# Kernel tuning notes

Hardware: AMD Instinct MI355X
Metric: run time of the kernel (lower is better)

The kernel has to match this reference:

```python
import jax, jax.numpy as jnp
import numpy as np

NUM_HEADS = 1
LN_EPS = 1e-5


def setup_inputs() -> dict:
    key = jax.random.key(0)
    ks = jax.random.split(key, 4)
    B, N, C = 16, 128 * 128 + 1, 64
    x = jax.random.normal(ks[0], (B, N, C), dtype=jnp.float32)
    Wq = jax.random.normal(ks[1], (C, C), dtype=jnp.float32) * 0.02
    Wkv = jax.random.normal(ks[2], (C, 2 * C), dtype=jnp.float32) * 0.02
    ln_g = jnp.ones((C,), dtype=jnp.float32)
    ln_b = jnp.zeros((C,), dtype=jnp.float32)
    Wp = jax.random.normal(ks[3], (C, C), dtype=jnp.float32) * 0.02
    bp = jnp.zeros((C,), dtype=jnp.float32)
    return {"x": x, "Wq": Wq, "Wkv": Wkv, "ln_g": ln_g, "ln_b": ln_b,
            "Wp": Wp, "bp": bp, "H": 128, "W": 128}


def _layernorm(x, g, b):
    mu = x.mean(-1, keepdims=True)
    var = ((x - mu) ** 2).mean(-1, keepdims=True)
    return (x - mu) * jax.lax.rsqrt(var + LN_EPS) * g + b


def reference(x, Wq, Wkv, ln_g, ln_b, Wp, bp, H, W):
    B, N, C = x.shape
    h = NUM_HEADS
    d = C // h
    scale = d ** (-0.5)

    # remove weight token
    tokens = x[:, 1:, :]          # [B, N-1, C]
    wt = x[:, :1, :]              # [B, 1, C]

    # mask-gated selection: feat @ wt_token^T -> sigmoid -> binary mask
    mask_weight = jnp.einsum('bnc,bmc->bnm', tokens, wt)   # [B, N-1, 1]
    mask_prob = jax.nn.sigmoid(mask_weight)
    mask = (mask_prob > 0.5).astype(x.dtype)
    mask_count = mask.sum(axis=(1, 2))                      # [B]
    # if a batch element has an all-zero mask, set it to all-ones
    mask = jnp.where((mask_count == 0)[:, None, None], jnp.ones_like(mask), mask)

    # queries over the full sequence (with wt token)
    q = (x @ Wq).reshape(B, N, h, d).transpose(0, 2, 1, 3)  # [B, h, N, d]

    # simFeats_fusion: masked weighted-sum pooling into 2 tokens
    x_po_f = (tokens * mask * (mask_weight * mask)).sum(axis=1, keepdims=True)        # [B,1,C]
    x_ne_f = (tokens * (1 - mask) * (mask_weight * (1 - mask))).sum(axis=1, keepdims=True)
    x_ = jnp.concatenate([wt, x_po_f, x_ne_f], axis=1)      # [B, 3, C]
    x_ = _layernorm(x_, ln_g, ln_b)

    kv = (x_ @ Wkv).reshape(B, 3, 2, h, d).transpose(2, 0, 3, 1, 4)  # [2, B, h, 3, d]
    k, v = kv[0], kv[1]

    attn = jnp.einsum('bhnd,bhmd->bhnm', q, k) * scale       # [B, h, N, 3]
    attn = jax.nn.softmax(attn, axis=-1)
    out = jnp.einsum('bhnm,bhmd->bhnd', attn, v)             # [B, h, N, d]
    out = out.transpose(0, 2, 1, 3).reshape(B, N, C)
    out = out @ Wp + bp
    return (out, mask, mask_prob)
```

## Files before the change

kernel.cpp:

```cpp
#include <hip/hip_runtime.h>
#include <cstddef>

#define BB 16
#define NN 16385
#define NT 16384
#define CC 64
#define P1B 64
#define P3B 64

typedef __attribute__((ext_vector_type(4))) float f4;

__global__ __launch_bounds__(256) void k_p1(
    const float* __restrict__ x, const float* __restrict__ Wq,
    const float* __restrict__ Wkv, const float* __restrict__ Wp,
    float* __restrict__ mask_out, float* __restrict__ prob_out,
    float* __restrict__ po_part, float* __restrict__ ne_part,
    float* __restrict__ cnt_part,
    float* __restrict__ M2t, float* __restrict__ M3)
{
  const int b = blockIdx.y, bx = blockIdx.x;
  const int tid = threadIdx.x, lane = tid & 63, wave = tid >> 6;

  if (b == BB) {
    const int c = bx, j = lane, q = wave;
    float s2 = 0.f, s3 = 0.f;
    #pragma unroll
    for (int dd = 0; dd < 16; ++dd) {
      const int d = q * 16 + dd;
      s2 += Wq[j * 64 + d] * Wkv[c * 128 + d];
      s3 += Wkv[c * 128 + 64 + d] * Wp[d * 64 + j];
    }
    __shared__ float t2[4][64], t3[4][64];
    t2[q][j] = s2; t3[q][j] = s3;
    __syncthreads();
    if (q == 0) {
      M2t[c * 64 + j] = t2[0][j] + t2[1][j] + t2[2][j] + t2[3][j];
      M3 [c * 64 + j] = t3[0][j] + t3[1][j] + t3[2][j] + t3[3][j];
    }
    return;
  }

  const int g = lane & 15, t = lane >> 4, c0 = g * 4;
  const float* xb = x + (size_t)b * NN * CC;
  const f4 wt4 = *reinterpret_cast<const f4*>(xb + c0);

  float apo[4] = {0.f, 0.f, 0.f, 0.f};
  float ane4[4] = {0.f, 0.f, 0.f, 0.f};
  float cntl = 0.f;

  for (int grp = bx * 4 + wave; grp < NT / 4; grp += P1B * 4) {
    const int n0 = grp * 4;
    const f4 xv = *reinterpret_cast<const f4*>(xb + (size_t)(1 + n0 + t) * CC + c0);
    float p = xv.x * wt4.x + xv.y * wt4.y + xv.z * wt4.z + xv.w * wt4.w;
    p += __shfl_xor(p, 1);
    p += __shfl_xor(p, 2);
    p += __shfl_xor(p, 4);
    p += __shfl_xor(p, 8);
    const bool m = p > 0.f;
    const float po = m ? p : 0.f;
    const float ne = m ? 0.f : p;
    apo[0] += po * xv.x; apo[1] += po * xv.y; apo[2] += po * xv.z; apo[3] += po * xv.w;
    ane4[0] += ne * xv.x; ane4[1] += ne * xv.y; ane4[2] += ne * xv.z; ane4[3] += ne * xv.w;
    if (g == 0) {
      const int nt = n0 + t;
      mask_out[(size_t)b * NT + nt] = m ? 1.f : 0.f;
      prob_out[(size_t)b * NT + nt] = 1.f / (1.f + __expf(-p));
      if (m) cntl += 1.f;
    }
  }

  #pragma unroll
  for (int i = 0; i < 4; ++i) {
    apo[i] += __shfl_xor(apo[i], 16); apo[i] += __shfl_xor(apo[i], 32);
    ane4[i] += __shfl_xor(ane4[i], 16); ane4[i] += __shfl_xor(ane4[i], 32);
  }
  cntl += __shfl_xor(cntl, 16);
  cntl += __shfl_xor(cntl, 32);

  __shared__ float s_po[4][64], s_ne[4][64], s_cnt[4];
  if (t == 0) {
    #pragma unroll
    for (int i = 0; i < 4; ++i) { s_po[wave][c0 + i] = apo[i]; s_ne[wave][c0 + i] = ane4[i]; }
  }
  if (lane == 0) s_cnt[wave] = cntl;
  __syncthreads();
  if (wave == 0) {
    const float sp = s_po[0][lane] + s_po[1][lane] + s_po[2][lane] + s_po[3][lane];
    const float sn = s_ne[0][lane] + s_ne[1][lane] + s_ne[2][lane] + s_ne[3][lane];
    const size_t base = ((size_t)b * P1B + bx) * 64 + lane;
    po_part[base] = sp;
    ne_part[base] = sn;
    if (lane == 0) cnt_part[b * P1B + bx] = s_cnt[0] + s_cnt[1] + s_cnt[2] + s_cnt[3];
  }
}

__global__ __launch_bounds__(256) void k_p23(
    const float* __restrict__ x, const float* __restrict__ ln_g,
    const float* __restrict__ ln_b, const float* __restrict__ bp,
    const float* __restrict__ po_part, const float* __restrict__ ne_part,
    const float* __restrict__ cnt_part,
    const float* __restrict__ M2t, const float* __restrict__ M3,
    float* __restrict__ out, float* __restrict__ mask_out)
{
  const int b = blockIdx.y;
  const int tid = threadIdx.x, lane = tid & 63, wave = tid >> 6;
  const int j = lane, q = wave;
  const int kq = tid >> 4, jg = tid & 15;
  const float* xb = x + (size_t)b * NN * CC;

  __shared__ float s_flag;
  __shared__ f4 sm_po[16][16], sm_ne[16][16];
  __shared__ float po_s[64], ne_s[64];
  __shared__ float y[3][64];
  __shared__ float A_l[3][64], V_l[3][64];

  f4 sp4 = {0.f, 0.f, 0.f, 0.f}, sn4 = {0.f, 0.f, 0.f, 0.f};
  #pragma unroll
  for (int i = 0; i < 4; ++i) {
    const size_t base = ((size_t)b * P1B + kq + 16 * i) * 64 + jg * 4;
    const f4 a = *reinterpret_cast<const f4*>(po_part + base);
    const f4 c = *reinterpret_cast<const f4*>(ne_part + base);
    sp4 += a; sn4 += c;
  }
  sm_po[kq][jg] = sp4;
  sm_ne[kq][jg] = sn4;

  if (q == 3) {
    float cs = cnt_part[b * P1B + j];
    for (int o = 1; o < 64; o <<= 1) cs += __shfl_xor(cs, o);
    if (j == 0) s_flag = (cs == 0.f) ? 1.f : 0.f;
  }
  __syncthreads();

  if (q == 0) {
    float s1 = 0.f, s2v = 0.f;
    #pragma unroll
    for (int k = 0; k < 16; ++k) {
      s1  += sm_po[k][j >> 2][j & 3];
      s2v += sm_ne[k][j >> 2][j & 3];
    }
    po_s[j] = s1; ne_s[j] = s2v;
  }
  __syncthreads();

  const bool flag = (s_flag != 0.f);
  if (q < 3) {
    float v;
    if (q == 0)      v = xb[j];
    else if (q == 1) v = flag ? ne_s[j] : po_s[j];
    else             v = flag ? 0.f : ne_s[j];
    float s = v;
    for (int o = 1; o < 64; o <<= 1) s += __shfl_xor(s, o);
    const float mu = s * (1.f / 64.f);
    const float d = v - mu;
    float s2 = d * d;
    for (int o = 1; o < 64; o <<= 1) s2 += __shfl_xor(s2, o);
    y[q][j] = d * rsqrtf(s2 * (1.f / 64.f) + 1e-5f) * ln_g[j] + ln_b[j];
  }
  __syncthreads();

  if (q < 3) {
    float sa = 0.f, sv = 0.f;
    #pragma unroll 8
    for (int c = 0; c < 64; ++c) {
      const float yc = y[q][c];
      sa += yc * M2t[c * 64 + j];
      sv += yc * M3 [c * 64 + j];
    }
    A_l[q][j] = 0.125f * sa;
    V_l[q][j] = sv;
  }
  __syncthreads();

  const int r = lane >> 3, c0 = (lane & 7) * 8;
  const f4 A0a = *reinterpret_cast<const f4*>(&A_l[0][c0]);
  const f4 A0b = *reinterpret_cast<const f4*>(&A_l[0][c0 + 4]);
  const f4 A1a = *reinterpret_cast<const f4*>(&A_l[1][c0]);
  const f4 A1b = *reinterpret_cast<const f4*>(&A_l[1][c0 + 4]);
  const f4 A2a = *reinterpret_cast<const f4*>(&A_l[2][c0]);
  const f4 A2b = *reinterpret_cast<const f4*>(&A_l[2][c0 + 4]);
  const f4 V0a = *reinterpret_cast<const f4*>(&V_l[0][c0]);
  const f4 V0b = *reinterpret_cast<const f4*>(&V_l[0][c0 + 4]);
  const f4 V1a = *reinterpret_cast<const f4*>(&V_l[1][c0]);
  const f4 V1b = *reinterpret_cast<const f4*>(&V_l[1][c0 + 4]);
  const f4 V2a = *reinterpret_cast<const f4*>(&V_l[2][c0]);
  const f4 V2b = *reinterpret_cast<const f4*>(&V_l[2][c0 + 4]);
  const f4 BPa = *reinterpret_cast<const f4*>(bp + c0);
  const f4 BPb = *reinterpret_cast<const f4*>(bp + c0 + 4);

  if (flag) {
    for (int i = blockIdx.x * 256 + tid; i < NT; i += P3B * 256)
      mask_out[(size_t)b * NT + i] = 1.f;
  }

  float* ob = out + (size_t)b * NN * CC;

  const int ngroups = (NN + 7) / 8;
  for (int grp = blockIdx.x * 4 + wave; grp < ngroups; grp += P3B * 4) {
    const int n = grp * 8 + r;
    const bool valid = n < NN;
    f4 x0 = {0.f, 0.f, 0.f, 0.f}, x1 = {0.f, 0.f, 0.f, 0.f};
    if (valid) {
      x0 = *reinterpret_cast<const f4*>(xb + (size_t)n * CC + c0);
      x1 = *reinterpret_cast<const f4*>(xb + (size_t)n * CC + c0 + 4);
    }

    float p0 = x0.x * A0a.x + x0.y * A0a.y + x0.z * A0a.z + x0.w * A0a.w
             + x1.x * A0b.x + x1.y * A0b.y + x1.z * A0b.z + x1.w * A0b.w;
    float p1 = x0.x * A1a.x + x0.y * A1a.y + x0.z * A1a.z + x0.w * A1a.w
             + x1.x * A1b.x + x1.y * A1b.y + x1.z * A1b.z + x1.w * A1b.w;
    float p2 = x0.x * A2a.x + x0.y * A2a.y + x0.z * A2a.z + x0.w * A2a.w
             + x1.x * A2b.x + x1.y * A2b.y + x1.z * A2b.z + x1.w * A2b.w;
    #pragma unroll
    for (int o = 1; o < 8; o <<= 1) {
      p0 += __shfl_xor(p0, o);
      p1 += __shfl_xor(p1, o);
      p2 += __shfl_xor(p2, o);
    }
    const float mx = fmaxf(p0, fmaxf(p1, p2));
    float e0 = __expf(p0 - mx), e1 = __expf(p1 - mx), e2 = __expf(p2 - mx);
    const float inv = 1.f / (e0 + e1 + e2);
    e0 *= inv; e1 *= inv; e2 *= inv;

    f4 o0, o1;
    o0.x = BPa.x + e0 * V0a.x + e1 * V1a.x + e2 * V2a.x;
    o0.y = BPa.y + e0 * V0a.y + e1 * V1a.y + e2 * V2a.y;
    o0.z = BPa.z + e0 * V0a.z + e1 * V1a.z + e2 * V2a.z;
    o0.w = BPa.w + e0 * V0a.w + e1 * V1a.w + e2 * V2a.w;
    o1.x = BPb.x + e0 * V0b.x + e1 * V1b.x + e2 * V2b.x;
    o1.y = BPb.y + e0 * V0b.y + e1 * V1b.y + e2 * V2b.y;
    o1.z = BPb.z + e0 * V0b.z + e1 * V1b.z + e2 * V2b.z;
    o1.w = BPb.w + e0 * V0b.w + e1 * V1b.w + e2 * V2b.w;
    if (valid) {
      *reinterpret_cast<f4*>(ob + (size_t)n * CC + c0) = o0;
      *reinterpret_cast<f4*>(ob + (size_t)n * CC + c0 + 4) = o1;
    }
  }
}

extern "C" void kernel_launch(void* const* d_in, const int* in_sizes, int n_in,
                              void* d_out, int out_size, void* d_ws, size_t ws_size,
                              hipStream_t stream) {
  (void)in_sizes; (void)n_in; (void)out_size; (void)ws_size;
  const float* x    = (const float*)d_in[0];
  const float* Wq   = (const float*)d_in[1];
  const float* Wkv  = (const float*)d_in[2];
  const float* ln_g = (const float*)d_in[3];
  const float* ln_b = (const float*)d_in[4];
  const float* Wp   = (const float*)d_in[5];
  const float* bp   = (const float*)d_in[6];

  float* out      = (float*)d_out;
  float* mask_out = out + (size_t)BB * NN * CC;
  float* prob_out = mask_out + (size_t)BB * NT;

  float* ws        = (float*)d_ws;
  float* po_part   = ws;
  float* ne_part   = po_part + (size_t)BB * P1B * 64;
  float* cnt_part  = ne_part + (size_t)BB * P1B * 64;
  float* M2t       = cnt_part + BB * P1B;
  float* M3        = M2t + 64 * 64;

  k_p1<<<dim3(P1B, BB + 1), 256, 0, stream>>>(x, Wq, Wkv, Wp, mask_out, prob_out,
                                              po_part, ne_part, cnt_part, M2t, M3);
  k_p23<<<dim3(P3B, BB), 256, 0, stream>>>(x, ln_g, ln_b, bp,
                                           po_part, ne_part, cnt_part,
                                           M2t, M3, out, mask_out);
}
```

Measured before the change: 44.83 us.

## Fuse two phases into one cooperative kernel with a grid-wide sync

Merges the masked-pooling phase and the attention/projection phase into a single cooperative kernel that separates them with a grid barrier. The weight-product matrices are computed by designated blocks instead of an extra block row. This removes the second kernel launch and the gap between launches, and may let x stay warmer in cache for the second pass. The cost is the grid sync and a hard limit on grid size from co-residency, with a fallback to the two-kernel path if the cooperative launch fails.

```diff
diff --git a/kernel.cpp b/kernel.cpp
--- a/kernel.cpp
+++ b/kernel.cpp
@@ -1,5 +1,8 @@
 #include <hip/hip_runtime.h>
+#include <hip/hip_cooperative_groups.h>
 #include <cstddef>
+
+namespace cg = cooperative_groups;
 
 #define BB 16
 #define NN 16385
@@ -7,8 +10,227 @@
 #define CC 64
 #define P1B 64
 #define P3B 64
+#define PSTRIDE 64
 
 typedef __attribute__((ext_vector_type(4))) float f4;
+
+template <int PB>
+__global__ __launch_bounds__(256, 4) void k_fused(
+    const float* __restrict__ x, const float* __restrict__ Wq,
+    const float* __restrict__ Wkv, const float* __restrict__ ln_g,
+    const float* __restrict__ ln_b, const float* __restrict__ Wp,
+    const float* __restrict__ bp,
+    float* __restrict__ out, float* __restrict__ mask_out,
+    float* __restrict__ prob_out,
+    float* __restrict__ po_part, float* __restrict__ ne_part,
+    float* __restrict__ cnt_part,
+    float* __restrict__ M2t, float* __restrict__ M3)
+{
+  const int bid = blockIdx.x;
+  const int b = bid / PB, bx = bid % PB;
+  const int tid = threadIdx.x, lane = tid & 63, wave = tid >> 6;
+  const float* xb = x + (size_t)b * NN * CC;
+
+  __shared__ float s_po[4][64], s_ne[4][64], s_cnt[4];
+  __shared__ float s_flag;
+  __shared__ f4 sm_po[16][16], sm_ne[16][16];
+  __shared__ float po_s[64], ne_s[64];
+  __shared__ float y[3][64];
+  __shared__ float A_l[3][64], V_l[3][64];
+
+  {
+    const int g = lane & 15, t = lane >> 4, c0 = g * 4;
+    const f4 wt4 = *reinterpret_cast<const f4*>(xb + c0);
+
+    float apo[4] = {0.f, 0.f, 0.f, 0.f};
+    float ane4[4] = {0.f, 0.f, 0.f, 0.f};
+    float cntl = 0.f;
+
+    for (int grp = bx * 4 + wave; grp < NT / 4; grp += PB * 4) {
+      const int n0 = grp * 4;
+      const f4 xv = *reinterpret_cast<const f4*>(xb + (size_t)(1 + n0 + t) * CC + c0);
+      float p = xv.x * wt4.x + xv.y * wt4.y + xv.z * wt4.z + xv.w * wt4.w;
+      p += __shfl_xor(p, 1);
+      p += __shfl_xor(p, 2);
+      p += __shfl_xor(p, 4);
+      p += __shfl_xor(p, 8);
+      const bool m = p > 0.f;
+      const float po = m ? p : 0.f;
+      const float ne = m ? 0.f : p;
+      apo[0] += po * xv.x; apo[1] += po * xv.y; apo[2] += po * xv.z; apo[3] += po * xv.w;
+      ane4[0] += ne * xv.x; ane4[1] += ne * xv.y; ane4[2] += ne * xv.z; ane4[3] += ne * xv.w;
+      if (g == 0) {
+        const int nt = n0 + t;
+        mask_out[(size_t)b * NT + nt] = m ? 1.f : 0.f;
+        prob_out[(size_t)b * NT + nt] = 1.f / (1.f + __expf(-p));
+        if (m) cntl += 1.f;
+      }
+    }
+
+    #pragma unroll
+    for (int i = 0; i < 4; ++i) {
+      apo[i] += __shfl_xor(apo[i], 16); apo[i] += __shfl_xor(apo[i], 32);
+      ane4[i] += __shfl_xor(ane4[i], 16); ane4[i] += __shfl_xor(ane4[i], 32);
+    }
+    cntl += __shfl_xor(cntl, 16);
+    cntl += __shfl_xor(cntl, 32);
+
+    if (t == 0) {
+      #pragma unroll
+      for (int i = 0; i < 4; ++i) { s_po[wave][c0 + i] = apo[i]; s_ne[wave][c0 + i] = ane4[i]; }
+    }
+    if (lane == 0) s_cnt[wave] = cntl;
+    __syncthreads();
+    if (wave == 0) {
+      const float sp = s_po[0][lane] + s_po[1][lane] + s_po[2][lane] + s_po[3][lane];
+      const float sn = s_ne[0][lane] + s_ne[1][lane] + s_ne[2][lane] + s_ne[3][lane];
+      const size_t base = ((size_t)b * PSTRIDE + bx) * 64 + lane;
+      po_part[base] = sp;
+      ne_part[base] = sn;
+      if (lane == 0) cnt_part[b * PSTRIDE + bx] = s_cnt[0] + s_cnt[1] + s_cnt[2] + s_cnt[3];
+    }
+
+    if (bx == 1) {
+      const int j = tid & 63, cc = tid >> 6;
+      const int c = 4 * b + cc;
+      float s2 = 0.f, s3 = 0.f;
+      #pragma unroll 8
+      for (int d = 0; d < 64; ++d) {
+        s2 += Wq[j * 64 + d] * Wkv[c * 128 + d];
+        s3 += Wkv[c * 128 + 64 + d] * Wp[d * 64 + j];
+      }
+      M2t[c * 64 + j] = s2;
+      M3 [c * 64 + j] = s3;
+    }
+  }
+
+  cg::this_grid().sync();
+
+  const int j = lane, q = wave;
+  const int kq = tid >> 4, jg = tid & 15;
+
+  f4 sp4 = {0.f, 0.f, 0.f, 0.f}, sn4 = {0.f, 0.f, 0.f, 0.f};
+  #pragma unroll
+  for (int k = kq; k < PB; k += 16) {
+    const size_t base = ((size_t)b * PSTRIDE + k) * 64 + jg * 4;
+    sp4 += *reinterpret_cast<const f4*>(po_part + base);
+    sn4 += *reinterpret_cast<const f4*>(ne_part + base);
+  }
+  sm_po[kq][jg] = sp4;
+  sm_ne[kq][jg] = sn4;
+
+  if (q == 3) {
+    float cs = (j < PB) ? cnt_part[b * PSTRIDE + j] : 0.f;
+    for (int o = 1; o < 64; o <<= 1) cs += __shfl_xor(cs, o);
+    if (j == 0) s_flag = (cs == 0.f) ? 1.f : 0.f;
+  }
+  __syncthreads();
+
+  if (q == 0) {
+    float s1 = 0.f, s2v = 0.f;
+    #pragma unroll
+    for (int k = 0; k < 16; ++k) {
+      s1  += sm_po[k][j >> 2][j & 3];
+      s2v += sm_ne[k][j >> 2][j & 3];
+    }
+    po_s[j] = s1; ne_s[j] = s2v;
+  }
+  __syncthreads();
+
+  const bool flag = (s_flag != 0.f);
+  if (q < 3) {
+    float v;
+    if (q == 0)      v = xb[j];
+    else if (q == 1) v = flag ? ne_s[j] : po_s[j];
+    else             v = flag ? 0.f : ne_s[j];
+    float s = v;
+    for (int o = 1; o < 64; o <<= 1) s += __shfl_xor(s, o);
+    const float mu = s * (1.f / 64.f);
+    const float d = v - mu;
+    float s2 = d * d;
+    for (int o = 1; o < 64; o <<= 1) s2 += __shfl_xor(s2, o);
+    y[q][j] = d * rsqrtf(s2 * (1.f / 64.f) + 1e-5f) * ln_g[j] + ln_b[j];
+  }
+  __syncthreads();
+
+  if (q < 3) {
+    float sa = 0.f, sv = 0.f;
+    #pragma unroll 8
+    for (int c = 0; c < 64; ++c) {
+      const float yc = y[q][c];
+      sa += yc * M2t[c * 64 + j];
+      sv += yc * M3 [c * 64 + j];
+    }
+    A_l[q][j] = 0.125f * sa;
+    V_l[q][j] = sv;
+  }
+  __syncthreads();
+
+  const int r = lane >> 3, c0 = (lane & 7) * 8;
+  const f4 A0a = *reinterpret_cast<const f4*>(&A_l[0][c0]);
+  const f4 A0b = *reinterpret_cast<const f4*>(&A_l[0][c0 + 4]);
+  const f4 A1a = *reinterpret_cast<const f4*>(&A_l[1][c0]);
+  const f4 A1b = *reinterpret_cast<const f4*>(&A_l[1][c0 + 4]);
+  const f4 A2a = *reinterpret_cast<const f4*>(&A_l[2][c0]);
+  const f4 A2b = *reinterpret_cast<const f4*>(&A_l[2][c0 + 4]);
+  const f4 V0a = *reinterpret_cast<const f4*>(&V_l[0][c0]);
+  const f4 V0b = *reinterpret_cast<const f4*>(&V_l[0][c0 + 4]);
+  const f4 V1a = *reinterpret_cast<const f4*>(&V_l[1][c0]);
+  const f4 V1b = *reinterpret_cast<const f4*>(&V_l[1][c0 + 4]);
+  const f4 V2a = *reinterpret_cast<const f4*>(&V_l[2][c0]);
+  const f4 V2b = *reinterpret_cast<const f4*>(&V_l[2][c0 + 4]);
+  const f4 BPa = *reinterpret_cast<const f4*>(bp + c0);
+  const f4 BPb = *reinterpret_cast<const f4*>(bp + c0 + 4);
+
+  if (flag) {
+    for (int i = bx * 256 + tid; i < NT; i += PB * 256)
+      mask_out[(size_t)b * NT + i] = 1.f;
+  }
+
+  float* ob = out + (size_t)b * NN * CC;
+
+  const int ngroups = (NN + 7) / 8;
+  for (int grp = bx * 4 + wave; grp < ngroups; grp += PB * 4) {
+    const int n = grp * 8 + r;
+    const bool valid = n < NN;
+    f4 x0 = {0.f, 0.f, 0.f, 0.f}, x1 = {0.f, 0.f, 0.f, 0.f};
+    if (valid) {
+      const f4* p = reinterpret_cast<const f4*>(xb + (size_t)n * CC + c0);
+      x0 = p[0]; x1 = p[1];
+    }
+
+    float p0 = x0.x * A0a.x + x0.y * A0a.y + x0.z * A0a.z + x0.w * A0a.w
+             + x1.x * A0b.x + x1.y * A0b.y + x1.z * A0b.z + x1.w * A0b.w;
+    float p1 = x0.x * A1a.x + x0.y * A1a.y + x0.z * A1a.z + x0.w * A1a.w
+             + x1.x * A1b.x + x1.y * A1b.y + x1.z * A1b.z + x1.w * A1b.w;
+    float p2 = x0.x * A2a.x + x0.y * A2a.y + x0.z * A2a.z + x0.w * A2a.w
+             + x1.x * A2b.x + x1.y * A2b.y + x1.z * A2b.z + x1.w * A2b.w;
+    #pragma unroll
+    for (int o = 1; o < 8; o <<= 1) {
+      p0 += __shfl_xor(p0, o);
+      p1 += __shfl_xor(p1, o);
+      p2 += __shfl_xor(p2, o);
+    }
+    const float mx = fmaxf(p0, fmaxf(p1, p2));
+    float e0 = __expf(p0 - mx), e1 = __expf(p1 - mx), e2 = __expf(p2 - mx);
+    const float inv = 1.f / (e0 + e1 + e2);
+    e0 *= inv; e1 *= inv; e2 *= inv;
+
+    f4 o0, o1;
+    o0.x = BPa.x + e0 * V0a.x + e1 * V1a.x + e2 * V2a.x;
+    o0.y = BPa.y + e0 * V0a.y + e1 * V1a.y + e2 * V2a.y;
+    o0.z = BPa.z + e0 * V0a.z + e1 * V1a.z + e2 * V2a.z;
+    o0.w = BPa.w + e0 * V0a.w + e1 * V1a.w + e2 * V2a.w;
+    o1.x = BPb.x + e0 * V0b.x + e1 * V1b.x + e2 * V2b.x;
+    o1.y = BPb.y + e0 * V0b.y + e1 * V1b.y + e2 * V2b.y;
+    o1.z = BPb.z + e0 * V0b.z + e1 * V1b.z + e2 * V2b.z;
+    o1.w = BPb.w + e0 * V0b.w + e1 * V1b.w + e2 * V2b.w;
+    if (valid) {
+      f4* p = reinterpret_cast<f4*>(ob + (size_t)n * CC + c0);
+      p[0] = o0; p[1] = o1;
+    }
+  }
+}
 
 __global__ __launch_bounds__(256) void k_p1(
     const float* __restrict__ x, const float* __restrict__ Wq,
@@ -87,14 +309,14 @@
   if (wave == 0) {
     const float sp = s_po[0][lane] + s_po[1][lane] + s_po[2][lane] + s_po[3][lane];
     const float sn = s_ne[0][lane] + s_ne[1][lane] + s_ne[2][lane] + s_ne[3][lane];
-    const size_t base = ((size_t)b * P1B + bx) * 64 + lane;
+    const size_t base = ((size_t)b * PSTRIDE + bx) * 64 + lane;
     po_part[base] = sp;
     ne_part[base] = sn;
-    if (lane == 0) cnt_part[b * P1B + bx] = s_cnt[0] + s_cnt[1] + s_cnt[2] + s_cnt[3];
+    if (lane == 0) cnt_part[b * PSTRIDE + bx] = s_cnt[0] + s_cnt[1] + s_cnt[2] + s_cnt[3];
   }
 }
 
-__global__ __launch_bounds__(256) void k_p23(
+__global__ __launch_bounds__(256, 4) void k_p23(
     const float* __restrict__ x, const float* __restrict__ ln_g,
     const float* __restrict__ ln_b, const float* __restrict__ bp,
     const float* __restrict__ po_part, const float* __restrict__ ne_part,
@@ -117,16 +339,15 @@
   f4 sp4 = {0.f, 0.f, 0.f, 0.f}, sn4 = {0.f, 0.f, 0.f, 0.f};
   #pragma unroll
   for (int i = 0; i < 4; ++i) {
-    const size_t base = ((size_t)b * P1B + kq + 16 * i) * 64 + jg * 4;
-    const f4 a = *reinterpret_cast<const f4*>(po_part + base);
-    const f4 c = *reinterpret_cast<const f4*>(ne_part + base);
-    sp4 += a; sn4 += c;
+    const size_t base = ((size_t)b * PSTRIDE + kq + 16 * i) * 64 + jg * 4;
+    sp4 += *reinterpret_cast<const f4*>(po_part + base);
+    sn4 += *reinterpret_cast<const f4*>(ne_part + base);
   }
   sm_po[kq][jg] = sp4;
   sm_ne[kq][jg] = sn4;
 
   if (q == 3) {
-    float cs = cnt_part[b * P1B + j];
+    float cs = cnt_part[b * PSTRIDE + j];
     for (int o = 1; o < 64; o <<= 1) cs += __shfl_xor(cs, o);
     if (j == 0) s_flag = (cs == 0.f) ? 1.f : 0.f;
   }
@@ -201,8 +422,8 @@
     const bool valid = n < NN;
     f4 x0 = {0.f, 0.f, 0.f, 0.f}, x1 = {0.f, 0.f, 0.f, 0.f};
     if (valid) {
-      x0 = *reinterpret_cast<const f4*>(xb + (size_t)n * CC + c0);
-      x1 = *reinterpret_cast<const f4*>(xb + (size_t)n * CC + c0 + 4);
+      const f4* p = reinterpret_cast<const f4*>(xb + (size_t)n * CC + c0);
+      x0 = p[0]; x1 = p[1];
     }
 
     float p0 = x0.x * A0a.x + x0.y * A0a.y + x0.z * A0a.z + x0.w * A0a.w
@@ -232,8 +453,8 @@
     o1.z = BPb.z + e0 * V0b.z + e1 * V1b.z + e2 * V2b.z;
     o1.w = BPb.w + e0 * V0b.w + e1 * V1b.w + e2 * V2b.w;
     if (valid) {
-      *reinterpret_cast<f4*>(ob + (size_t)n * CC + c0) = o0;
-      *reinterpret_cast<f4*>(ob + (size_t)n * CC + c0 + 4) = o1;
+      f4* p = reinterpret_cast<f4*>(ob + (size_t)n * CC + c0);
+      p[0] = o0; p[1] = o1;
     }
   }
 }
@@ -256,14 +477,42 @@
 
   float* ws        = (float*)d_ws;
   float* po_part   = ws;
-  float* ne_part   = po_part + (size_t)BB * P1B * 64;
-  float* cnt_part  = ne_part + (size_t)BB * P1B * 64;
-  float* M2t       = cnt_part + BB * P1B;
+  float* ne_part   = po_part + (size_t)BB * PSTRIDE * 64;
+  float* cnt_part  = ne_part + (size_t)BB * PSTRIDE * 64;
+  float* M2t       = cnt_part + BB * PSTRIDE;
   float* M3        = M2t + 64 * 64;
 
-  k_p1<<<dim3(P1B, BB + 1), 256, 0, stream>>>(x, Wq, Wkv, Wp, mask_out, prob_out,
-                                              po_part, ne_part, cnt_part, M2t, M3);
-  k_p23<<<dim3(P3B, BB), 256, 0, stream>>>(x, ln_g, ln_b, bp,
-                                           po_part, ne_part, cnt_part,
-                                           M2t, M3, out, mask_out);
+  int maxBlk = 0;
+  hipError_t qerr = hipOccupancyMaxActiveBlocksPerMultiprocessor(
+      &maxBlk, (const void*)k_fused<64>, 256, 0);
+
+  bool launched = false;
+  if (qerr == hipSuccess && maxBlk >= 2) {
+    void* args[] = {
+      (void*)&x, (void*)&Wq, (void*)&Wkv, (void*)&ln_g, (void*)&ln_b,
+      (void*)&Wp, (void*)&bp, (void*)&out, (void*)&mask_out, (void*)&prob_out,
+      (void*)&po_part, (void*)&ne_part, (void*)&cnt_part, (void*)&M2t, (void*)&M3
+    };
+    hipError_t lerr;
+    if (maxBlk >= 4) {
+      lerr = hipLaunchCooperativeKernel((const void*)k_fused<64>, dim3(BB * 64),
+                                        dim3(256), args, 0, stream);
+    } else if (maxBlk == 3) {
+      lerr = hipLaunchCooperativeKernel((const void*)k_fused<48>, dim3(BB * 48),
+                                        dim3(256), args, 0, stream);
+    } else {
+      lerr = hipLaunchCooperativeKernel((const void*)k_fused<32>, dim3(BB * 32),
+                                        dim3(256), args, 0, stream);
+    }
+    launched = (lerr == hipSuccess);
+    if (!launched) (void)hipGetLastError();
+  }
+
+  if (!launched) {
+    k_p1<<<dim3(P1B, BB + 1), 256, 0, stream>>>(x, Wq, Wkv, Wp, mask_out, prob_out,
+                                                po_part, ne_part, cnt_part, M2t, M3);
+    k_p23<<<dim3(P3B, BB), 256, 0, stream>>>(x, ln_g, ln_b, bp,
+                                             po_part, ne_part, cnt_part,
+                                             M2t, M3, out, mask_out);
+  }
 }
```

New measurement: 115.2 us. 157% more time.
